# Performance work log

Measured on AMD Instinct MI355X. Metric: run time of the kernel, lower is better.

The kernel has to match this reference:

```python
import jax, jax.numpy as jnp
import numpy as np

N_NODES = 50000
N_EDGES = 400000
IN_DIM = 512
OUT_DIM = 512


def setup_inputs() -> dict:
    key = jax.random.key(0)
    k1, k2, k3, k4 = jax.random.split(key, 4)
    x = jax.random.normal(k1, (N_NODES, IN_DIM), dtype=jnp.float32)
    edge_index = jax.random.randint(k2, (2, N_EDGES), 0, N_NODES, dtype=jnp.int64)
    # nn.Linear(in_dim, out_dim): weight [out, in], bias [out]
    W = jax.random.normal(k3, (OUT_DIM, IN_DIM), dtype=jnp.float32) / np.sqrt(IN_DIM)
    b = jax.random.normal(k4, (OUT_DIM,), dtype=jnp.float32) * 0.01
    return {"x": x, "edge_index": edge_index, "W": W, "b": b}


def reference(x, edge_index, W, b):
    n = x.shape[0]
    loops = jnp.arange(n, dtype=edge_index.dtype)
    row = jnp.concatenate([edge_index[0], loops])  # src
    col = jnp.concatenate([edge_index[1], loops])  # dst
    # degree from row counts (matches torch.bincount(row)); self-loops ensure deg >= 1
    deg = jax.ops.segment_sum(jnp.ones(row.shape[0], dtype=x.dtype), row, num_segments=n)
    dis = jax.lax.rsqrt(deg)  # deg^-0.5
    norm = dis[row] * dis[col]  # [E+N]
    h = x @ W.T + b  # [N, out_dim]
    # out[dst] += norm * h[src], fused gather-scale-scatter
    out = jax.ops.segment_sum(norm[:, None] * h[row], col, num_segments=n)
    return jax.nn.relu(out)
```

## Files before the change

### kernel.cpp

```cpp
#include <hip/hip_runtime.h>
#include <hip/hip_bf16.h>

#define K_DIM 512
#define N_DIM 512

typedef __attribute__((ext_vector_type(8))) short s8v;
typedef __attribute__((ext_vector_type(4))) short s4v;
typedef __attribute__((ext_vector_type(4))) float f4v;

__device__ __forceinline__ short f2bf(float f) {
  union { float f; unsigned u; } v; v.f = f;
  unsigned r = (v.u + 0x7FFFu + ((v.u >> 16) & 1u)) >> 16;
  return (short)r;
}
__device__ __forceinline__ float bflo(unsigned u) {
  union { unsigned u; float f; } v; v.u = u << 16; return v.f;
}
__device__ __forceinline__ float bfhi(unsigned u) {
  union { unsigned u; float f; } v; v.u = u & 0xffff0000u; return v.f;
}

__device__ __forceinline__ void gload16(const void* g, void* l) {
  __builtin_amdgcn_global_load_lds(
      (const __attribute__((address_space(1))) void*)g,
      (__attribute__((address_space(3))) void*)l, 16, 0, 0);
}

__device__ __forceinline__ int edge_stride(const int* __restrict__ e32, int lane) {
  int chk = e32[2 * lane + 1];
  unsigned long long m = __ballot(chk == 0);
  return (m == ~0ULL) ? 2 : 1;
}

__global__ __launch_bounds__(256) void k_pre1(const float* __restrict__ W,
    short* __restrict__ Wb, const int* __restrict__ e32, int* __restrict__ outdeg,
    int* __restrict__ indeg, int E, int nbw) {
  int b = blockIdx.x;
  int t = threadIdx.x;
  if (b < nbw) {
    int i = (b * 256 + t) * 4;
    float4 f = *(const float4*)(W + i);
    s4v s; s[0] = f2bf(f.x); s[1] = f2bf(f.y); s[2] = f2bf(f.z); s[3] = f2bf(f.w);
    *(s4v*)(Wb + i) = s;
  } else {
    int st = edge_stride(e32, t & 63);
    int i = (b - nbw) * 256 + t;
    if (i < E) {
      int r = e32[(size_t)i * st];
      int c = e32[(size_t)(E + i) * st];
      atomicAdd(&outdeg[r], 1);
      atomicAdd(&indeg[c], 1);
    }
  }
}

__global__ __launch_bounds__(256) void k_pre2(const int* __restrict__ outdeg,
    float* __restrict__ dis, const int* __restrict__ indeg, int* __restrict__ part,
    int n, int nbd) {
  int b = blockIdx.x;
  if (b < nbd) {
    int i = b * 256 + threadIdx.x;
    if (i < n) dis[i] = rsqrtf((float)(outdeg[i] + 1));
  } else {
    __shared__ int sm[256];
    int lb = b - nbd;
    int i = lb * 256 + threadIdx.x;
    sm[threadIdx.x] = (i < n) ? indeg[i] : 0;
    __syncthreads();
    for (int off = 128; off > 0; off >>= 1) {
      if (threadIdx.x < off) sm[threadIdx.x] += sm[threadIdx.x + off];
      __syncthreads();
    }
    if (threadIdx.x == 0) part[lb] = sm[0];
  }
}

__global__ void k_scan_b(int* __restrict__ part, int nb, int* __restrict__ row_start, int n) {
  __shared__ int sm[256];
  int t = threadIdx.x;
  int v = (t < nb) ? part[t] : 0;
  sm[t] = v; __syncthreads();
  for (int off = 1; off < 256; off <<= 1) {
    int a = (t >= off) ? sm[t - off] : 0;
    __syncthreads();
    sm[t] += a;
    __syncthreads();
  }
  part[t] = sm[t] - v;
  if (t == 255) row_start[n] = sm[255];
}

__global__ void k_scan_c(const int* __restrict__ in, const int* __restrict__ part,
                         int* __restrict__ row_start, int* __restrict__ cursor, int n) {
  __shared__ int sm[256];
  int i = blockIdx.x * 256 + threadIdx.x;
  int v = (i < n) ? in[i] : 0;
  sm[threadIdx.x] = v; __syncthreads();
  for (int off = 1; off < 256; off <<= 1) {
    int a = (threadIdx.x >= off) ? sm[threadIdx.x - off] : 0;
    __syncthreads();
    sm[threadIdx.x] += a;
    __syncthreads();
  }
  if (i < n) {
    int excl = part[blockIdx.x] + sm[threadIdx.x] - v;
    row_start[i] = excl;
    cursor[i] = excl;
  }
}

__global__ void k_fill(const int* __restrict__ e32, int* __restrict__ cursor,
                       int* __restrict__ csr, int E) {
  int st = edge_stride(e32, threadIdx.x & 63);
  int i = blockIdx.x * blockDim.x + threadIdx.x;
  if (i >= E) return;
  int r = e32[(size_t)i * st];
  int c = e32[(size_t)(E + i) * st];
  int p = atomicAdd(&cursor[c], 1);
  csr[p] = r;
}

__global__ __launch_bounds__(256) void k_convXS(const float* __restrict__ x,
    const float* __restrict__ dis, short* __restrict__ xs, long long total) {
  long long i = ((long long)blockIdx.x * 256 + threadIdx.x) * 8;
  if (i >= total) return;
  float dv = dis[i >> 9];
  float4 f0 = *(const float4*)(x + i);
  float4 f1 = *(const float4*)(x + i + 4);
  s8v v;
  v[0] = f2bf(dv * f0.x); v[1] = f2bf(dv * f0.y);
  v[2] = f2bf(dv * f0.z); v[3] = f2bf(dv * f0.w);
  v[4] = f2bf(dv * f1.x); v[5] = f2bf(dv * f1.y);
  v[6] = f2bf(dv * f1.z); v[7] = f2bf(dv * f1.w);
  *(s8v*)(xs + i) = v;
}

__device__ __forceinline__ void add8(float* acc, uint4 rv) {
  acc[0] += bflo(rv.x); acc[1] += bfhi(rv.x);
  acc[2] += bflo(rv.y); acc[3] += bfhi(rv.y);
  acc[4] += bflo(rv.z); acc[5] += bfhi(rv.z);
  acc[6] += bflo(rv.w); acc[7] += bfhi(rv.w);
}

__global__ __launch_bounds__(256) void k_agg(const short* __restrict__ xs,
    const float* __restrict__ dis, const int* __restrict__ row_start,
    const int* __restrict__ csr, short* __restrict__ xa, float* __restrict__ s,
    int n) {
  int wid = blockIdx.x * 4 + (threadIdx.x >> 6);
  int nw = gridDim.x * 4;
  int lane = threadIdx.x & 63;
  const short* hl = xs + lane * 8;
  for (int v = wid; v < n; v += nw) {
    float acc[8];
    float accs = 0.f;
    {
      uint4 r = *(const uint4*)(hl + (size_t)v * N_DIM);
      acc[0] = bflo(r.x); acc[1] = bfhi(r.x);
      acc[2] = bflo(r.y); acc[3] = bfhi(r.y);
      acc[4] = bflo(r.z); acc[5] = bfhi(r.z);
      acc[6] = bflo(r.w); acc[7] = bfhi(r.w);
    }
    int sb = __builtin_amdgcn_readfirstlane(row_start[v]);
    int eb = __builtin_amdgcn_readfirstlane(row_start[v + 1]);
    int idx = sb;
    for (; idx + 8 <= eb; idx += 8) {
      int s0 = csr[idx],     s1 = csr[idx + 1], s2 = csr[idx + 2], s3 = csr[idx + 3];
      int s4 = csr[idx + 4], s5 = csr[idx + 5], s6 = csr[idx + 6], s7 = csr[idx + 7];
      uint4 r0 = *(const uint4*)(hl + (size_t)s0 * N_DIM);
      uint4 r1 = *(const uint4*)(hl + (size_t)s1 * N_DIM);
      uint4 r2 = *(const uint4*)(hl + (size_t)s2 * N_DIM);
      uint4 r3 = *(const uint4*)(hl + (size_t)s3 * N_DIM);
      uint4 r4 = *(const uint4*)(hl + (size_t)s4 * N_DIM);
      uint4 r5 = *(const uint4*)(hl + (size_t)s5 * N_DIM);
      uint4 r6 = *(const uint4*)(hl + (size_t)s6 * N_DIM);
      uint4 r7 = *(const uint4*)(hl + (size_t)s7 * N_DIM);
      accs += dis[s0] + dis[s1] + dis[s2] + dis[s3]
            + dis[s4] + dis[s5] + dis[s6] + dis[s7];
      add8(acc, r0); add8(acc, r1); add8(acc, r2); add8(acc, r3);
      add8(acc, r4); add8(acc, r5); add8(acc, r6); add8(acc, r7);
    }
    for (; idx + 4 <= eb; idx += 4) {
      int s0 = csr[idx], s1 = csr[idx + 1], s2 = csr[idx + 2], s3 = csr[idx + 3];
      uint4 r0 = *(const uint4*)(hl + (size_t)s0 * N_DIM);
      uint4 r1 = *(const uint4*)(hl + (size_t)s1 * N_DIM);
      uint4 r2 = *(const uint4*)(hl + (size_t)s2 * N_DIM);
      uint4 r3 = *(const uint4*)(hl + (size_t)s3 * N_DIM);
      accs += dis[s0] + dis[s1] + dis[s2] + dis[s3];
      add8(acc, r0); add8(acc, r1); add8(acc, r2); add8(acc, r3);
    }
    for (; idx < eb; ++idx) {
      int s0 = csr[idx];
      uint4 r0 = *(const uint4*)(hl + (size_t)s0 * N_DIM);
      accs += dis[s0];
      add8(acc, r0);
    }
    float dv = dis[v];
    s8v o;
    #pragma unroll
    for (int q = 0; q < 8; ++q) o[q] = f2bf(dv * acc[q]);
    *(s8v*)(xa + (size_t)v * N_DIM + lane * 8) = o;
    if (lane == 0) s[v] = dv * (accs + dv);
  }
}

__global__ __launch_bounds__(256, 3) void k_gemm(const short* __restrict__ xa,
    const short* __restrict__ Wb, const float* __restrict__ bias,
    const float* __restrict__ s, float* __restrict__ out, int M) {
  __shared__ __align__(16) short As[2][128 * 32];
  __shared__ __align__(16) short Bs[2][128 * 32];
  __shared__ __align__(16) float Es[4][16][68];
  int nwg = gridDim.x;
  int orig = blockIdx.x;
  int q8 = nwg >> 3, r8 = nwg & 7;
  int xcd = orig & 7, pos = orig >> 3;
  int swz = (xcd < r8 ? xcd * (q8 + 1) : r8 * (q8 + 1) + (xcd - r8) * q8) + pos;
  const int n0 = (swz & 3) * 128;
  const int m0 = (swz >> 2) * 128;

  const int tid = threadIdx.x;
  const int lane = tid & 63;
  const int wv = tid >> 6, wr = wv >> 1, wc = wv & 1;
  const int la = lane & 15, lg = lane >> 4;

  const short* ag[2];
  const short* bg[2];
  int doff[2];
  #pragma unroll
  for (int r = 0; r < 2; ++r) {
    int id = r * 256 + tid;
    int row = id >> 2;
    int ch = id & 3;
    int arow = m0 + row; if (arow >= M) arow = M - 1;
    ag[r] = xa + (size_t)arow * K_DIM + ch * 8;
    bg[r] = Wb + (size_t)(n0 + row) * K_DIM + ch * 8;
    doff[r] = (r * 256 + (tid & 192)) * 16;
  }
  int aro[4], bro[4];
  #pragma unroll
  for (int i = 0; i < 4; ++i) {
    aro[i] = (64 * wr + 16 * i + la) * 64 + lg * 16;
    bro[i] = (64 * wc + 16 * i + la) * 64 + lg * 16;
  }

  f4v acc[4][4] = {};

  #pragma unroll
  for (int r = 0; r < 2; ++r) {
    gload16(ag[r], (char*)As + doff[r]);
    gload16(bg[r], (char*)Bs + doff[r]);
  }
  __syncthreads();

  for (int kt = 0; kt < 16; ++kt) {
    const int cur = kt & 1;
    const int nxt = cur ^ 1;
    if (kt < 15) {
      const int kk = (kt + 1) * 32;
      #pragma unroll
      for (int r = 0; r < 2; ++r) {
        gload16(ag[r] + kk, (char*)As + nxt * 8192 + doff[r]);
        gload16(bg[r] + kk, (char*)Bs + nxt * 8192 + doff[r]);
      }
    }
    s8v af[4], bf[4];
    const char* ab = (const char*)As + cur * 8192;
    const char* bb = (const char*)Bs + cur * 8192;
    #pragma unroll
    for (int i = 0; i < 4; ++i) af[i] = *(const s8v*)(ab + aro[i]);
    #pragma unroll
    for (int j = 0; j < 4; ++j) bf[j] = *(const s8v*)(bb + bro[j]);
    #pragma unroll
    for (int i = 0; i < 4; ++i)
      #pragma unroll
      for (int j = 0; j < 4; ++j)
        acc[i][j] = __builtin_amdgcn_mfma_f32_16x16x32_bf16(af[i], bf[j], acc[i][j], 0, 0, 0);
    __syncthreads();
  }

  float bv[4];
  #pragma unroll
  for (int j = 0; j < 4; ++j) bv[j] = bias[n0 + 64 * wc + 16 * j + la];
  #pragma unroll
  for (int i = 0; i < 4; ++i) {
    int rowb = m0 + 64 * wr + 16 * i + lg * 4;
    float sv[4];
    #pragma unroll
    for (int r = 0; r < 4; ++r) sv[r] = (rowb + r < M) ? s[rowb + r] : 0.f;
    #pragma unroll
    for (int j = 0; j < 4; ++j)
      #pragma unroll
      for (int r = 0; r < 4; ++r)
        Es[wv][lg * 4 + r][16 * j + la] = fmaxf(acc[i][j][r] + sv[r] * bv[j], 0.f);
    __builtin_amdgcn_s_waitcnt(0);
    int gr0 = m0 + 64 * wr + 16 * i;
    #pragma unroll
    for (int rr = 0; rr < 4; ++rr) {
      int id = rr * 64 + lane;
      int rl = id >> 4, ch = id & 15;
      f4v val = *(const f4v*)&Es[wv][rl][ch * 4];
      if (gr0 + rl < M)
        __builtin_nontemporal_store(val,
            (f4v*)(out + (size_t)(gr0 + rl) * N_DIM + n0 + 64 * wc + ch * 4));
    }
    __builtin_amdgcn_s_waitcnt(0);
  }
}

extern "C" void kernel_launch(void* const* d_in, const int* in_sizes, int n_in,
                              void* d_out, int out_size, void* d_ws, size_t ws_size,
                              hipStream_t stream) {
  const float* x = (const float*)d_in[0];
  const int* e32 = (const int*)d_in[1];
  const float* W = (const float*)d_in[2];
  const float* bias = (const float*)d_in[3];
  float* out = (float*)d_out;
  int M = in_sizes[0] / K_DIM;
  int E = in_sizes[1] / 2;

  char* ws = (char*)d_ws;
  size_t off = 0;
  auto alloc = [&](size_t bytes) {
    void* p = ws + off;
    off = (off + bytes + 255) & ~(size_t)255;
    return p;
  };
  short* Wb      = (short*)alloc((size_t)N_DIM * K_DIM * 2);
  short* xa      = (short*)alloc((size_t)M * N_DIM * 2);
  float* dis     = (float*)alloc((size_t)M * 4);
  float* sարr    = nullptr;
  float* sv      = (float*)alloc((size_t)M * 4);
  int*   outdeg  = (int*)alloc((size_t)M * 4);
  int*   indeg   = (int*)alloc((size_t)M * 4);
  int*   rstart  = (int*)alloc((size_t)(M + 1) * 4);
  int*   cursor  = (int*)alloc((size_t)M * 4);
  int*   part    = (int*)alloc(256 * 4);
  int*   csr     = (int*)alloc((size_t)E * 4);
  if (off > ws_size) return;

  short* xs = (short*)d_out;

  (void)hipMemsetAsync(outdeg, 0, (size_t)M * 4, stream);
  (void)hipMemsetAsync(indeg, 0, (size_t)M * 4, stream);

  int nbw = N_DIM * K_DIM / 4 / 256;
  int nbh = (E + 255) / 256;
  k_pre1<<<nbw + nbh, 256, 0, stream>>>(W, Wb, e32, outdeg, indeg, E, nbw);
  int nscan = (M + 255) / 256;
  k_pre2<<<nscan * 2, 256, 0, stream>>>(outdeg, dis, indeg, part, M, nscan);
  k_scan_b<<<1, 256, 0, stream>>>(part, nscan, rstart, M);
  k_scan_c<<<nscan, 256, 0, stream>>>(indeg, part, rstart, cursor, M);
  k_fill<<<nbh, 256, 0, stream>>>(e32, cursor, csr, E);
  long long totalx = (long long)M * K_DIM;
  k_convXS<<<(int)((totalx / 8 + 255) / 256), 256, 0, stream>>>(x, dis, xs, totalx);
  k_agg<<<2048, 256, 0, stream>>>(xs, dis, rstart, csr, xa, sv, M);
  int nmc = (M + 127) / 128;
  k_gemm<<<nmc * 4, 256, 0, stream>>>(xa, Wb, bias, sv, out, M);
}
```

Baseline: 218.2 us.

## Merge scan kernels, fuse CSR fill with x conversion, raise GEMM occupancy

Each block now scans the 196 partial sums redundantly, which folds the two scan kernels into one. The CSR fill and the x-to-bf16 scaling are merged into one launch by splitting on block index, and the two memsets become one. The GEMM reuses its A/B shared buffers for the epilogue staging, which cuts LDS from about 49KB to 32KB. Its launch bounds go from 3 to 5 waves per SIMD, and the full waitcnt is narrowed to lgkmcnt only. Together these cut launch count and allow more resident GEMM workgroups, at the cost of register pressure and redundant scan work.

New measurement: 217.9 us. No clear change (-0.2%).

```diff
diff --git a/kernel.cpp b/kernel.cpp
--- a/kernel.cpp
+++ b/kernel.cpp
@@ -75,64 +75,68 @@
   }
 }
 
-__global__ void k_scan_b(int* __restrict__ part, int nb, int* __restrict__ row_start, int n) {
+__global__ __launch_bounds__(256) void k_scan(const int* __restrict__ indeg,
+    const int* __restrict__ part, int* __restrict__ row_start,
+    int* __restrict__ cursor, int n, int nb) {
+  __shared__ int sp[256];
   __shared__ int sm[256];
-  int t = threadIdx.x;
-  int v = (t < nb) ? part[t] : 0;
-  sm[t] = v; __syncthreads();
+  int t = threadIdx.x, b = blockIdx.x;
+  sp[t] = (t < nb) ? part[t] : 0;
+  __syncthreads();
+  for (int off = 1; off < 256; off <<= 1) {
+    int a = (t >= off) ? sp[t - off] : 0;
+    __syncthreads();
+    sp[t] += a;
+    __syncthreads();
+  }
+  int pOff = (b > 0) ? sp[b - 1] : 0;
+  if (b == 0 && t == 255) row_start[n] = sp[255];
+  int i = b * 256 + t;
+  int v = (i < n) ? indeg[i] : 0;
+  sm[t] = v;
+  __syncthreads();
   for (int off = 1; off < 256; off <<= 1) {
     int a = (t >= off) ? sm[t - off] : 0;
     __syncthreads();
     sm[t] += a;
     __syncthreads();
   }
-  part[t] = sm[t] - v;
-  if (t == 255) row_start[n] = sm[255];
-}
-
-__global__ void k_scan_c(const int* __restrict__ in, const int* __restrict__ part,
-                         int* __restrict__ row_start, int* __restrict__ cursor, int n) {
-  __shared__ int sm[256];
-  int i = blockIdx.x * 256 + threadIdx.x;
-  int v = (i < n) ? in[i] : 0;
-  sm[threadIdx.x] = v; __syncthreads();
-  for (int off = 1; off < 256; off <<= 1) {
-    int a = (threadIdx.x >= off) ? sm[threadIdx.x - off] : 0;
-    __syncthreads();
-    sm[threadIdx.x] += a;
-    __syncthreads();
-  }
   if (i < n) {
-    int excl = part[blockIdx.x] + sm[threadIdx.x] - v;
+    int excl = pOff + sm[t] - v;
     row_start[i] = excl;
     cursor[i] = excl;
   }
 }
 
-__global__ void k_fill(const int* __restrict__ e32, int* __restrict__ cursor,
-                       int* __restrict__ csr, int E) {
-  int st = edge_stride(e32, threadIdx.x & 63);
-  int i = blockIdx.x * blockDim.x + threadIdx.x;
-  if (i >= E) return;
-  int r = e32[(size_t)i * st];
-  int c = e32[(size_t)(E + i) * st];
-  int p = atomicAdd(&cursor[c], 1);
-  csr[p] = r;
-}
-
-__global__ __launch_bounds__(256) void k_convXS(const float* __restrict__ x,
-    const float* __restrict__ dis, short* __restrict__ xs, long long total) {
-  long long i = ((long long)blockIdx.x * 256 + threadIdx.x) * 8;
-  if (i >= total) return;
-  float dv = dis[i >> 9];
-  float4 f0 = *(const float4*)(x + i);
-  float4 f1 = *(const float4*)(x + i + 4);
-  s8v v;
-  v[0] = f2bf(dv * f0.x); v[1] = f2bf(dv * f0.y);
-  v[2] = f2bf(dv * f0.z); v[3] = f2bf(dv * f0.w);
-  v[4] = f2bf(dv * f1.x); v[5] = f2bf(dv * f1.y);
-  v[6] = f2bf(dv * f1.z); v[7] = f2bf(dv * f1.w);
-  *(s8v*)(xs + i) = v;
+__global__ __launch_bounds__(256) void k_fillconv(const int* __restrict__ e32,
+    int* __restrict__ cursor, int* __restrict__ csr, int E,
+    const float* __restrict__ x, const float* __restrict__ dis,
+    short* __restrict__ xs, long long totalx, int nbh) {
+  int b = blockIdx.x;
+  int t = threadIdx.x;
+  if (b < nbh) {
+    int st = edge_stride(e32, t & 63);
+    int i = b * 256 + t;
+    if (i < E) {
+      int r = e32[(size_t)i * st];
+      int c = e32[(size_t)(E + i) * st];
+      int p = atomicAdd(&cursor[c], 1);
+      csr[p] = r;
+    }
+  } else {
+    long long i = ((long long)(b - nbh) * 256 + t) * 8;
+    if (i < totalx) {
+      float dv = dis[i >> 9];
+      float4 f0 = *(const float4*)(x + i);
+      float4 f1 = *(const float4*)(x + i + 4);
+      s8v v;
+      v[0] = f2bf(dv * f0.x); v[1] = f2bf(dv * f0.y);
+      v[2] = f2bf(dv * f0.z); v[3] = f2bf(dv * f0.w);
+      v[4] = f2bf(dv * f1.x); v[5] = f2bf(dv * f1.y);
+      v[6] = f2bf(dv * f1.z); v[7] = f2bf(dv * f1.w);
+      *(s8v*)(xs + i) = v;
+    }
+  }
 }
 
 __device__ __forceinline__ void add8(float* acc, uint4 rv) {
@@ -203,12 +207,12 @@
   }
 }
 
-__global__ __launch_bounds__(256, 3) void k_gemm(const short* __restrict__ xa,
+__global__ __launch_bounds__(256, 5) void k_gemm(const short* __restrict__ xa,
     const short* __restrict__ Wb, const float* __restrict__ bias,
     const float* __restrict__ s, float* __restrict__ out, int M) {
-  __shared__ __align__(16) short As[2][128 * 32];
-  __shared__ __align__(16) short Bs[2][128 * 32];
-  __shared__ __align__(16) float Es[4][16][68];
+  __shared__ __align__(16) char smem[32768];
+  short* As = (short*)smem;
+  short* Bs = (short*)(smem + 16384);
   int nwg = gridDim.x;
   int orig = blockIdx.x;
   int q8 = nwg >> 3, r8 = nwg & 7;
@@ -277,6 +281,7 @@
     __syncthreads();
   }
 
+  float* Es = (float*)(smem + wv * 4352);
   float bv[4];
   #pragma unroll
   for (int j = 0; j < 4; ++j) bv[j] = bias[n0 + 64 * wc + 16 * j + la];
@@ -290,19 +295,19 @@
     for (int j = 0; j < 4; ++j)
       #pragma unroll
       for (int r = 0; r < 4; ++r)
-        Es[wv][lg * 4 + r][16 * j + la] = fmaxf(acc[i][j][r] + sv[r] * bv[j], 0.f);
-    __builtin_amdgcn_s_waitcnt(0);
+        Es[(lg * 4 + r) * 68 + 16 * j + la] = fmaxf(acc[i][j][r] + sv[r] * bv[j], 0.f);
+    asm volatile("s_waitcnt lgkmcnt(0)" ::: "memory");
     int gr0 = m0 + 64 * wr + 16 * i;
     #pragma unroll
     for (int rr = 0; rr < 4; ++rr) {
       int id = rr * 64 + lane;
       int rl = id >> 4, ch = id & 15;
-      f4v val = *(const f4v*)&Es[wv][rl][ch * 4];
+      f4v val = *(const f4v*)&Es[rl * 68 + ch * 4];
       if (gr0 + rl < M)
         __builtin_nontemporal_store(val,
             (f4v*)(out + (size_t)(gr0 + rl) * N_DIM + n0 + 64 * wc + ch * 4));
     }
-    __builtin_amdgcn_s_waitcnt(0);
+    asm volatile("s_waitcnt lgkmcnt(0)" ::: "memory");
   }
 }
 
@@ -327,7 +332,6 @@
   short* Wb      = (short*)alloc((size_t)N_DIM * K_DIM * 2);
   short* xa      = (short*)alloc((size_t)M * N_DIM * 2);
   float* dis     = (float*)alloc((size_t)M * 4);
-  float* sարr    = nullptr;
   float* sv      = (float*)alloc((size_t)M * 4);
   int*   outdeg  = (int*)alloc((size_t)M * 4);
   int*   indeg   = (int*)alloc((size_t)M * 4);
@@ -339,19 +343,19 @@
 
   short* xs = (short*)d_out;
 
-  (void)hipMemsetAsync(outdeg, 0, (size_t)M * 4, stream);
-  (void)hipMemsetAsync(indeg, 0, (size_t)M * 4, stream);
+  size_t zbytes = (size_t)((char*)indeg - (char*)outdeg) + (size_t)M * 4;
+  (void)hipMemsetAsync(outdeg, 0, zbytes, stream);
 
   int nbw = N_DIM * K_DIM / 4 / 256;
   int nbh = (E + 255) / 256;
   k_pre1<<<nbw + nbh, 256, 0, stream>>>(W, Wb, e32, outdeg, indeg, E, nbw);
   int nscan = (M + 255) / 256;
   k_pre2<<<nscan * 2, 256, 0, stream>>>(outdeg, dis, indeg, part, M, nscan);
-  k_scan_b<<<1, 256, 0, stream>>>(part, nscan, rstart, M);
-  k_scan_c<<<nscan, 256, 0, stream>>>(indeg, part, rstart, cursor, M);
-  k_fill<<<nbh, 256, 0, stream>>>(e32, cursor, csr, E);
+  k_scan<<<nscan, 256, 0, stream>>>(indeg, part, rstart, cursor, M, nscan);
   long long totalx = (long long)M * K_DIM;
-  k_convXS<<<(int)((totalx / 8 + 255) / 256), 256, 0, stream>>>(x, dis, xs, totalx);
+  int nbx = (int)((totalx / 8 + 255) / 256);
+  k_fillconv<<<nbh + nbx, 256, 0, stream>>>(e32, cursor, csr, E, x, dis, xs,
+                                            totalx, nbh);
   k_agg<<<2048, 256, 0, stream>>>(xs, dis, rstart, csr, xa, sv, M);
   int nmc = (M + 127) / 128;
   k_gemm<<<nmc * 4, 256, 0, stream>>>(xa, Wb, bias, sv, out, M);
```
